# Optimization experiments

Hardware: AMD Instinct MI355X
Metric: run time of the kernel (lower is better)

Reference implementation:

```python
import jax, jax.numpy as jnp
import numpy as np

S, N, D, F, E = 2048, 8, 1024, 4096, 8
STD = 0.02


def setup_inputs() -> dict:
    key = jax.random.key(0)
    ks = jax.random.split(key, 5)
    x = jax.random.normal(ks[0], (S, N, D), dtype=jnp.float32)
    Wg = jax.random.normal(ks[1], (E, D), dtype=jnp.float32) * STD
    W1 = jax.random.normal(ks[2], (E, F, D), dtype=jnp.float32) * STD
    b1 = jnp.zeros((E, F), dtype=jnp.float32)
    W2 = jax.random.normal(ks[3], (E, D, F), dtype=jnp.float32) * STD
    b2 = jnp.zeros((E, D), dtype=jnp.float32)
    return {"x": x, "Wg": Wg, "W1": W1, "b1": b1, "W2": W2, "b2": b2}


def reference(x, Wg, W1, b1, W2, b2):
    # Gate (eval mode: no gating noise). scores: [S, N, E]
    scores = jnp.einsum('snd,ed->sne', x, Wg)
    prob = jax.nn.softmax(scores, axis=-1)
    top1_idx = jnp.argmax(prob, axis=-1)                                   # [S, N] int
    top1_prob = jnp.take_along_axis(prob, top1_idx[..., None], axis=-1)[..., 0]  # [S, N]

    y = jnp.zeros_like(x)
    n_experts = Wg.shape[0]
    for e in range(n_experts):  # small fixed loop over experts
        h = jax.nn.gelu(jnp.einsum('snd,fd->snf', x, W1[e]) + b1[e], approximate=False)
        ye = jnp.einsum('snf,df->snd', h, W2[e]) + b2[e]
        mask = (top1_idx == e)[..., None]                                  # [S, N, 1]
        y = y + jnp.where(mask, ye * top1_prob[..., None], 0.0)
    return y
```

## Files before the change

### kernel.cpp

```cpp
#include <hip/hip_runtime.h>

#define S_TOK 16384
#define D_DIM 1024
#define F_DIM 4096
#define E_NUM 8

#define BM 256
#define BN 128
#define BK 64
#define MT_MAX 72

typedef short bf16x8 __attribute__((ext_vector_type(8)));
typedef float f32x4 __attribute__((ext_vector_type(4)));
typedef unsigned short ushort_t;

static __device__ __forceinline__ unsigned short f32_bf16(float f) {
  unsigned u = __float_as_uint(f);
  return (unsigned short)((u + 0x7FFFu + ((u >> 16) & 1u)) >> 16);
}

static __device__ __forceinline__ unsigned int pack_bf16x2(float a, float b) {
  unsigned ua = __float_as_uint(a);
  unsigned ub = __float_as_uint(b);
  unsigned lo = (ua + 0x7FFFu + ((ua >> 16) & 1u)) >> 16;
  unsigned hi = (ub + 0x7FFFu + ((ub >> 16) & 1u)) & 0xFFFF0000u;
  return lo | hi;
}

static __device__ __forceinline__ uint2 cvt_f4_bf4(const float4 v) {
  uint2 r;
  r.x = pack_bf16x2(v.x, v.y);
  r.y = pack_bf16x2(v.z, v.w);
  return r;
}

static __device__ __forceinline__ void load_lds16(const void* g, void* l) {
  __builtin_amdgcn_global_load_lds(g, l, 16, 0, 0);
}

static __device__ __forceinline__ float gelu_f(float v) {
  const float u = fabsf(v) * 0.70710678118654752f;
  const float t = 1.0f / (1.0f + 0.3275911f * u);
  const float poly = t * (0.254829592f + t * (-0.284496736f + t * (1.421413741f +
                     t * (-1.453152027f + t * 1.061405429f))));
  const float erfa = 1.0f - poly * __expf(-u * u);
  const float erfv = (v >= 0.0f) ? erfa : -erfa;
  return 0.5f * v * (1.0f + erfv);
}

__global__ void zero_counts_kernel(int* counts) {
  if (threadIdx.x < E_NUM) counts[threadIdx.x] = 0;
}

__global__ void cast2_kernel(const float* __restrict__ w1, ushort_t* __restrict__ o1,
                             const float* __restrict__ w2, ushort_t* __restrict__ o2) {
  const int half = 16384;
  const float* src = (blockIdx.x < half) ? w1 : w2;
  ushort_t* dst = (blockIdx.x < half) ? o1 : o2;
  const int b = (blockIdx.x < half) ? blockIdx.x : (blockIdx.x - half);
  const size_t base = ((size_t)b * blockDim.x + threadIdx.x) * 8;
  const float4 v0 = *(const float4*)(src + base);
  const float4 v1 = *(const float4*)(src + base + 4);
  const uint2 a = cvt_f4_bf4(v0), c = cvt_f4_bf4(v1);
  uint4 w; w.x = a.x; w.y = a.y; w.z = c.x; w.w = c.y;
  *(uint4*)(dst + base) = w;
}

__global__ void gate_kernel(const float* __restrict__ x,
                            const float* __restrict__ Wg,
                            ushort_t* __restrict__ xbf,
                            float* __restrict__ prob,
                            int* __restrict__ counts,
                            int* __restrict__ tok_list) {
  const int wv = threadIdx.x >> 6;
  const int lane = threadIdx.x & 63;
  const int t = blockIdx.x * 4 + wv;
  const float* xr = x + (size_t)t * D_DIM;
  ushort_t* xb = xbf + (size_t)t * D_DIM;

  float acc[E_NUM];
#pragma unroll
  for (int e = 0; e < E_NUM; ++e) acc[e] = 0.0f;

#pragma unroll
  for (int i = 0; i < 4; ++i) {
    const int k = i * 256 + lane * 4;
    const float4 v = *(const float4*)(xr + k);
    *(uint2*)(xb + k) = cvt_f4_bf4(v);
#pragma unroll
    for (int e = 0; e < E_NUM; ++e) {
      const float4 w = *(const float4*)(Wg + e * D_DIM + k);
      acc[e] += v.x * w.x + v.y * w.y + v.z * w.z + v.w * w.w;
    }
  }
#pragma unroll
  for (int e = 0; e < E_NUM; ++e) {
#pragma unroll
    for (int off = 32; off > 0; off >>= 1)
      acc[e] += __shfl_xor(acc[e], off, 64);
  }
  if (lane == 0) {
    float m = acc[0]; int bi = 0;
#pragma unroll
    for (int e = 1; e < E_NUM; ++e) {
      if (acc[e] > m) { m = acc[e]; bi = e; }
    }
    float s = 0.0f;
#pragma unroll
    for (int e = 0; e < E_NUM; ++e) s += expf(acc[e] - m);
    prob[t] = 1.0f / s;
    int p = atomicAdd(&counts[bi], 1);
    tok_list[bi * S_TOK + p] = t;
  }
}

__global__ void plan_kernel(const int* __restrict__ counts, int* __restrict__ plan) {
  if (threadIdx.x == 0) {
    int t = 0;
    for (int e = 0; e < E_NUM; ++e) {
      const int nt = (counts[e] + BM - 1) / BM;
      for (int i = 0; i < nt; ++i) {
        plan[1 + t] = e;
        plan[1 + MT_MAX + t] = i * BM;
        ++t;
      }
    }
    plan[0] = t;
  }
}

template <int KDIM, int NDIM, int EPI>
__launch_bounds__(512, 3)
__global__ void ffn_kernel(const ushort_t* __restrict__ A,
                           const ushort_t* __restrict__ B,
                           const float* __restrict__ bias,
                           const float* __restrict__ prob,
                           const int* __restrict__ counts,
                           const int* __restrict__ tok_list,
                           const int* __restrict__ plan,
                           ushort_t* __restrict__ Hout,
                           float* __restrict__ out) {
  constexpr int NT = NDIM / BN;
  constexpr int NK = KDIM / BK;
  const int ntiles = plan[0];
  const int live = ntiles * NT;
  if (blockIdx.x >= live) return;
  const int q = live >> 3, r = live & 7;
  const int xcd = blockIdx.x & 7, idx = blockIdx.x >> 3;
  const int wg = (xcd < r ? xcd * (q + 1) : r * (q + 1) + (xcd - r) * q) + idx;
  const int tile = wg / NT;
  const int n0 = (wg % NT) * BN;
  const int e = plan[1 + tile];
  const int m0 = plan[1 + MT_MAX + tile];
  const int cnt = counts[e];

  __shared__ ushort_t As[BM * BK];
  __shared__ ushort_t Bs[BN * BK];

  const int tid = threadIdx.x;
  const int lane = tid & 63;
  const int w = tid >> 6;
  const int wr = (w >> 1) * 64;
  const int wc = (w & 1) * 64;
  const int l15 = lane & 15;
  const int l4  = lane >> 4;

  const int sub = lane >> 3;
  const int sslot = ((lane & 7) ^ sub) * 8;

  const size_t ebase = (size_t)e * S_TOK;
  const ushort_t* Be = B + (size_t)e * NDIM * KDIM;
  const ushort_t* pA[4];
#pragma unroll
  for (int j = 0; j < 4; ++j) {
    const int ra = m0 + w * 32 + j * 8 + sub;
    const int tok = (ra < cnt) ? tok_list[ebase + ra] : 0;
    pA[j] = A + (size_t)tok * KDIM + sslot;
  }
  const ushort_t* pB[2];
#pragma unroll
  for (int j = 0; j < 2; ++j)
    pB[j] = Be + (size_t)(n0 + w * 16 + j * 8 + sub) * KDIM + sslot;

  int oA[4][2], oB[4][2];
#pragma unroll
  for (int m = 0; m < 4; ++m) {
    const int rr = wr + m * 16 + l15;
#pragma unroll
    for (int kk = 0; kk < 2; ++kk)
      oA[m][kk] = rr * BK + (((kk * 4 + l4) ^ (rr & 7)) * 8);
  }
#pragma unroll
  for (int n = 0; n < 4; ++n) {
    const int rr = wc + n * 16 + l15;
#pragma unroll
    for (int kk = 0; kk < 2; ++kk)
      oB[n][kk] = rr * BK + (((kk * 4 + l4) ^ (rr & 7)) * 8);
  }

  f32x4 acc[4][4];
#pragma unroll
  for (int i = 0; i < 4; ++i)
#pragma unroll
    for (int j = 0; j < 4; ++j)
      acc[i][j] = (f32x4){0.f, 0.f, 0.f, 0.f};

  for (int t = 0; t < NK; ++t) {
    const int k0 = t * BK;
#pragma unroll
    for (int j = 0; j < 4; ++j)
      load_lds16(pA[j] + k0, &As[w * 2048 + j * 512]);
#pragma unroll
    for (int j = 0; j < 2; ++j)
      load_lds16(pB[j] + k0, &Bs[w * 1024 + j * 512]);
    __syncthreads();

#pragma unroll
    for (int kk = 0; kk < 2; ++kk) {
      bf16x8 a[4], b[4];
#pragma unroll
      for (int i = 0; i < 4; ++i) {
        a[i] = *(const bf16x8*)&As[oA[i][kk]];
        b[i] = *(const bf16x8*)&Bs[oB[i][kk]];
      }
#pragma unroll
      for (int mi = 0; mi < 4; ++mi)
#pragma unroll
        for (int ni = 0; ni < 4; ++ni)
          acc[mi][ni] = __builtin_amdgcn_mfma_f32_16x16x32_bf16(a[mi], b[ni], acc[mi][ni], 0, 0, 0);
    }

    __syncthreads();
  }

  const float* be = bias + (size_t)e * NDIM;
#pragma unroll
  for (int mi = 0; mi < 4; ++mi) {
#pragma unroll
    for (int rr = 0; rr < 4; ++rr) {
      const int slot = m0 + wr + mi * 16 + l4 * 4 + rr;
      if (slot >= cnt) continue;
      const int tok = tok_list[ebase + slot];
      if (EPI == 0) {
        ushort_t* hrow = Hout + (size_t)tok * NDIM;
#pragma unroll
        for (int ni = 0; ni < 4; ++ni) {
          const int col = n0 + wc + ni * 16 + l15;
          hrow[col] = f32_bf16(gelu_f(acc[mi][ni][rr] + be[col]));
        }
      } else {
        const float p = prob[tok];
        float* orow = out + (size_t)tok * NDIM;
#pragma unroll
        for (int ni = 0; ni < 4; ++ni) {
          const int col = n0 + wc + ni * 16 + l15;
          orow[col] = (acc[mi][ni][rr] + be[col]) * p;
        }
      }
    }
  }
}

extern "C" void kernel_launch(void* const* d_in, const int* in_sizes, int n_in,
                              void* d_out, int out_size, void* d_ws, size_t ws_size,
                              hipStream_t stream) {
  const float* x  = (const float*)d_in[0];
  const float* Wg = (const float*)d_in[1];
  const float* W1 = (const float*)d_in[2];
  const float* b1 = (const float*)d_in[3];
  const float* W2 = (const float*)d_in[4];
  const float* b2 = (const float*)d_in[5];
  float* out = (float*)d_out;

  const size_t MB = 1ull << 20;
  char* ws = (char*)d_ws;
  int* counts      = (int*)(ws);
  int* plan        = (int*)(ws + 4096);
  float* prob      = (float*)(ws + 64 * 1024);
  int* tok_list    = (int*)(ws + 128 * 1024);
  ushort_t* xbf    = (ushort_t*)(ws + 1 * MB);
  ushort_t* W1bf   = (ushort_t*)(ws + 33 * MB);
  ushort_t* W2bf   = (ushort_t*)(ws + 97 * MB);
  ushort_t* H      = (ushort_t*)(ws + 161 * MB);

  zero_counts_kernel<<<1, 64, 0, stream>>>(counts);
  gate_kernel<<<S_TOK / 4, 256, 0, stream>>>(x, Wg, xbf, prob, counts, tok_list);
  plan_kernel<<<1, 64, 0, stream>>>(counts, plan);

  cast2_kernel<<<32768, 256, 0, stream>>>(W1, W1bf, W2, W2bf);

  ffn_kernel<D_DIM, F_DIM, 0><<<(F_DIM / BN) * MT_MAX, 512, 0, stream>>>(
      xbf, W1bf, b1, nullptr, counts, tok_list, plan, H, nullptr);

  ffn_kernel<F_DIM, D_DIM, 1><<<(D_DIM / BN) * MT_MAX, 512, 0, stream>>>(
      H, W2bf, b2, prob, counts, tok_list, plan, nullptr, out);
}
```

Measured before the change: 722.5 us.

## Enlarge FFN tile to 256x256 and double-buffer LDS loads

Widens the N tile from 128 to 256 so each wave computes a 128x64 sub-tile with 32 accumulators, which raises arithmetic intensity per LDS byte. It also double-buffers A/B in LDS, prefetching the next K slice while MFMAs run on the current one, and drops one barrier per iteration. The cost is higher register and LDS use (occupancy hint lowered from 3 to 2 blocks), and fewer workgroups, which may hurt load balance across CUs.

```diff
diff --git a/kernel.cpp b/kernel.cpp
--- a/kernel.cpp
+++ b/kernel.cpp
@@ -6,7 +6,7 @@
 #define E_NUM 8
 
 #define BM 256
-#define BN 128
+#define BN 256
 #define BK 64
 #define MT_MAX 72
 
@@ -130,7 +130,7 @@
 }
 
 template <int KDIM, int NDIM, int EPI>
-__launch_bounds__(512, 3)
+__launch_bounds__(512, 2)
 __global__ void ffn_kernel(const ushort_t* __restrict__ A,
                            const ushort_t* __restrict__ B,
                            const float* __restrict__ bias,
@@ -154,14 +154,14 @@
   const int m0 = plan[1 + MT_MAX + tile];
   const int cnt = counts[e];
 
-  __shared__ ushort_t As[BM * BK];
-  __shared__ ushort_t Bs[BN * BK];
+  __shared__ ushort_t As[2][BM * BK];
+  __shared__ ushort_t Bs[2][BN * BK];
 
   const int tid = threadIdx.x;
   const int lane = tid & 63;
   const int w = tid >> 6;
-  const int wr = (w >> 1) * 64;
-  const int wc = (w & 1) * 64;
+  const int wr2 = (w >> 2) * 128;
+  const int wc4 = (w & 3) * 64;
   const int l15 = lane & 15;
   const int l4  = lane >> 4;
 
@@ -171,90 +171,96 @@
   const size_t ebase = (size_t)e * S_TOK;
   const ushort_t* Be = B + (size_t)e * NDIM * KDIM;
   const ushort_t* pA[4];
+  const ushort_t* pB[4];
 #pragma unroll
   for (int j = 0; j < 4; ++j) {
-    const int ra = m0 + w * 32 + j * 8 + sub;
+    const int ra = m0 + j * 64 + w * 8 + sub;
     const int tok = (ra < cnt) ? tok_list[ebase + ra] : 0;
     pA[j] = A + (size_t)tok * KDIM + sslot;
-  }
-  const ushort_t* pB[2];
-#pragma unroll
-  for (int j = 0; j < 2; ++j)
-    pB[j] = Be + (size_t)(n0 + w * 16 + j * 8 + sub) * KDIM + sslot;
-
-  int oA[4][2], oB[4][2];
-#pragma unroll
-  for (int m = 0; m < 4; ++m) {
-    const int rr = wr + m * 16 + l15;
+    pB[j] = Be + (size_t)(n0 + j * 64 + w * 8 + sub) * KDIM + sslot;
+  }
+
+  int oA[8][2], oB[4][2];
+#pragma unroll
+  for (int m = 0; m < 8; ++m) {
+    const int rr = wr2 + m * 16 + l15;
 #pragma unroll
     for (int kk = 0; kk < 2; ++kk)
       oA[m][kk] = rr * BK + (((kk * 4 + l4) ^ (rr & 7)) * 8);
   }
 #pragma unroll
   for (int n = 0; n < 4; ++n) {
-    const int rr = wc + n * 16 + l15;
+    const int rr = wc4 + n * 16 + l15;
 #pragma unroll
     for (int kk = 0; kk < 2; ++kk)
       oB[n][kk] = rr * BK + (((kk * 4 + l4) ^ (rr & 7)) * 8);
   }
 
-  f32x4 acc[4][4];
-#pragma unroll
-  for (int i = 0; i < 4; ++i)
+  f32x4 acc[8][4];
+#pragma unroll
+  for (int i = 0; i < 8; ++i)
 #pragma unroll
     for (int j = 0; j < 4; ++j)
       acc[i][j] = (f32x4){0.f, 0.f, 0.f, 0.f};
 
+#pragma unroll
+  for (int j = 0; j < 4; ++j) {
+    load_lds16(pA[j], &As[0][j * 4096 + w * 512]);
+    load_lds16(pB[j], &Bs[0][j * 4096 + w * 512]);
+  }
+  __syncthreads();
+
   for (int t = 0; t < NK; ++t) {
-    const int k0 = t * BK;
-#pragma unroll
-    for (int j = 0; j < 4; ++j)
-      load_lds16(pA[j] + k0, &As[w * 2048 + j * 512]);
-#pragma unroll
-    for (int j = 0; j < 2; ++j)
-      load_lds16(pB[j] + k0, &Bs[w * 1024 + j * 512]);
+    const int cb = t & 1;
+    if (t + 1 < NK) {
+      const int kn = (t + 1) * BK;
+      const int nb = cb ^ 1;
+#pragma unroll
+      for (int j = 0; j < 4; ++j) {
+        load_lds16(pA[j] + kn, &As[nb][j * 4096 + w * 512]);
+        load_lds16(pB[j] + kn, &Bs[nb][j * 4096 + w * 512]);
+      }
+    }
+
+#pragma unroll
+    for (int kk = 0; kk < 2; ++kk) {
+      bf16x8 a[8], b[4];
+#pragma unroll
+      for (int m = 0; m < 8; ++m) a[m] = *(const bf16x8*)&As[cb][oA[m][kk]];
+#pragma unroll
+      for (int n = 0; n < 4; ++n) b[n] = *(const bf16x8*)&Bs[cb][oB[n][kk]];
+#pragma unroll
+      for (int m = 0; m < 8; ++m)
+#pragma unroll
+        for (int n = 0; n < 4; ++n)
+          acc[m][n] = __builtin_amdgcn_mfma_f32_16x16x32_bf16(a[m], b[n], acc[m][n], 0, 0, 0);
+    }
+
     __syncthreads();
-
-#pragma unroll
-    for (int kk = 0; kk < 2; ++kk) {
-      bf16x8 a[4], b[4];
-#pragma unroll
-      for (int i = 0; i < 4; ++i) {
-        a[i] = *(const bf16x8*)&As[oA[i][kk]];
-        b[i] = *(const bf16x8*)&Bs[oB[i][kk]];
-      }
-#pragma unroll
-      for (int mi = 0; mi < 4; ++mi)
-#pragma unroll
-        for (int ni = 0; ni < 4; ++ni)
-          acc[mi][ni] = __builtin_amdgcn_mfma_f32_16x16x32_bf16(a[mi], b[ni], acc[mi][ni], 0, 0, 0);
-    }
-
-    __syncthreads();
   }
 
   const float* be = bias + (size_t)e * NDIM;
 #pragma unroll
-  for (int mi = 0; mi < 4; ++mi) {
+  for (int m = 0; m < 8; ++m) {
 #pragma unroll
     for (int rr = 0; rr < 4; ++rr) {
-      const int slot = m0 + wr + mi * 16 + l4 * 4 + rr;
+      const int slot = m0 + wr2 + m * 16 + l4 * 4 + rr;
       if (slot >= cnt) continue;
       const int tok = tok_list[ebase + slot];
       if (EPI == 0) {
         ushort_t* hrow = Hout + (size_t)tok * NDIM;
 #pragma unroll
-        for (int ni = 0; ni < 4; ++ni) {
-          const int col = n0 + wc + ni * 16 + l15;
-          hrow[col] = f32_bf16(gelu_f(acc[mi][ni][rr] + be[col]));
+        for (int n = 0; n < 4; ++n) {
+          const int col = n0 + wc4 + n * 16 + l15;
+          hrow[col] = f32_bf16(gelu_f(acc[m][n][rr] + be[col]));
         }
       } else {
         const float p = prob[tok];
         float* orow = out + (size_t)tok * NDIM;
 #pragma unroll
-        for (int ni = 0; ni < 4; ++ni) {
-          const int col = n0 + wc + ni * 16 + l15;
-          orow[col] = (acc[mi][ni][rr] + be[col]) * p;
+        for (int n = 0; n < 4; ++n) {
+          const int col = n0 + wc4 + n * 16 + l15;
+          orow[col] = (acc[m][n][rr] + be[col]) * p;
         }
       }
     }
```

Result: slower. 842.0 us (+16.5%).

## Double-buffer LDS tiles in FFN GEMMs and fold plan and zeroing kernels

Applied to the files above, without the earlier changes.

The expert FFN GEMM moves to a double-buffered LDS scheme with BK=32. Each iteration issues the global-to-LDS loads for the next K tile before running the MFMAs on the current one, so each K step needs one barrier instead of two. The separate counts-zeroing and plan kernels are removed: zeroing now happens inside the weight-cast kernel, and each GEMM block rebuilds the tile-to-expert mapping from the counts itself. This drops two tiny launches. The cost is a lower occupancy hint (launch bounds 3 to 2), half as much K work per barrier, and a leftover stray prologue load.

```diff
diff --git a/kernel.cpp b/kernel.cpp
--- a/kernel.cpp
+++ b/kernel.cpp
@@ -7,7 +7,7 @@
 
 #define BM 256
 #define BN 128
-#define BK 64
+#define BK 32
 #define MT_MAX 72
 
 typedef short bf16x8 __attribute__((ext_vector_type(8)));
@@ -48,12 +48,10 @@
   return 0.5f * v * (1.0f + erfv);
 }
 
-__global__ void zero_counts_kernel(int* counts) {
-  if (threadIdx.x < E_NUM) counts[threadIdx.x] = 0;
-}
-
 __global__ void cast2_kernel(const float* __restrict__ w1, ushort_t* __restrict__ o1,
-                             const float* __restrict__ w2, ushort_t* __restrict__ o2) {
+                             const float* __restrict__ w2, ushort_t* __restrict__ o2,
+                             int* __restrict__ counts) {
+  if (blockIdx.x == 0 && threadIdx.x < E_NUM) counts[threadIdx.x] = 0;
   const int half = 16384;
   const float* src = (blockIdx.x < half) ? w1 : w2;
   ushort_t* dst = (blockIdx.x < half) ? o1 : o2;
@@ -114,35 +112,26 @@
   }
 }
 
-__global__ void plan_kernel(const int* __restrict__ counts, int* __restrict__ plan) {
-  if (threadIdx.x == 0) {
-    int t = 0;
-    for (int e = 0; e < E_NUM; ++e) {
-      const int nt = (counts[e] + BM - 1) / BM;
-      for (int i = 0; i < nt; ++i) {
-        plan[1 + t] = e;
-        plan[1 + MT_MAX + t] = i * BM;
-        ++t;
-      }
-    }
-    plan[0] = t;
-  }
-}
+#define SWZ32(r) (((r) >> 1) & 3)
 
 template <int KDIM, int NDIM, int EPI>
-__launch_bounds__(512, 3)
+__launch_bounds__(512, 2)
 __global__ void ffn_kernel(const ushort_t* __restrict__ A,
                            const ushort_t* __restrict__ B,
                            const float* __restrict__ bias,
                            const float* __restrict__ prob,
                            const int* __restrict__ counts,
                            const int* __restrict__ tok_list,
-                           const int* __restrict__ plan,
                            ushort_t* __restrict__ Hout,
                            float* __restrict__ out) {
   constexpr int NT = NDIM / BN;
   constexpr int NK = KDIM / BK;
-  const int ntiles = plan[0];
+  int nt_e[E_NUM], ntiles = 0;
+#pragma unroll
+  for (int i = 0; i < E_NUM; ++i) {
+    nt_e[i] = (counts[i] + BM - 1) / BM;
+    ntiles += nt_e[i];
+  }
   const int live = ntiles * NT;
   if (blockIdx.x >= live) return;
   const int q = live >> 3, r = live & 7;
@@ -150,12 +139,16 @@
   const int wg = (xcd < r ? xcd * (q + 1) : r * (q + 1) + (xcd - r) * q) + idx;
   const int tile = wg / NT;
   const int n0 = (wg % NT) * BN;
-  const int e = plan[1 + tile];
-  const int m0 = plan[1 + MT_MAX + tile];
+  int e = 0, m0 = 0, accb = 0;
+#pragma unroll
+  for (int i = 0; i < E_NUM; ++i) {
+    if (tile >= accb && tile < accb + nt_e[i]) { e = i; m0 = (tile - accb) * BM; }
+    accb += nt_e[i];
+  }
   const int cnt = counts[e];
 
-  __shared__ ushort_t As[BM * BK];
-  __shared__ ushort_t Bs[BN * BK];
+  __shared__ ushort_t As[2][BM * BK];
+  __shared__ ushort_t Bs[2][BN * BK];
 
   const int tid = threadIdx.x;
   const int lane = tid & 63;
@@ -165,37 +158,31 @@
   const int l15 = lane & 15;
   const int l4  = lane >> 4;
 
-  const int sub = lane >> 3;
-  const int sslot = ((lane & 7) ^ sub) * 8;
+  const int srow = tid >> 2;
+  const int sslot = ((tid & 3) ^ SWZ32(srow)) * 8;
+  const int w256 = w * 256;
 
   const size_t ebase = (size_t)e * S_TOK;
   const ushort_t* Be = B + (size_t)e * NDIM * KDIM;
-  const ushort_t* pA[4];
-#pragma unroll
-  for (int j = 0; j < 4; ++j) {
-    const int ra = m0 + w * 32 + j * 8 + sub;
+  const ushort_t* pA[2];
+#pragma unroll
+  for (int j = 0; j < 2; ++j) {
+    const int ra = m0 + j * 128 + srow;
     const int tok = (ra < cnt) ? tok_list[ebase + ra] : 0;
     pA[j] = A + (size_t)tok * KDIM + sslot;
   }
-  const ushort_t* pB[2];
-#pragma unroll
-  for (int j = 0; j < 2; ++j)
-    pB[j] = Be + (size_t)(n0 + w * 16 + j * 8 + sub) * KDIM + sslot;
-
-  int oA[4][2], oB[4][2];
+  const ushort_t* pBr = Be + (size_t)(n0 + srow) * KDIM + sslot;
+
+  int oA[4], oB[4];
 #pragma unroll
   for (int m = 0; m < 4; ++m) {
     const int rr = wr + m * 16 + l15;
-#pragma unroll
-    for (int kk = 0; kk < 2; ++kk)
-      oA[m][kk] = rr * BK + (((kk * 4 + l4) ^ (rr & 7)) * 8);
+    oA[m] = rr * BK + ((l4 ^ SWZ32(rr)) * 8);
   }
 #pragma unroll
   for (int n = 0; n < 4; ++n) {
     const int rr = wc + n * 16 + l15;
-#pragma unroll
-    for (int kk = 0; kk < 2; ++kk)
-      oB[n][kk] = rr * BK + (((kk * 4 + l4) ^ (rr & 7)) * 8);
+    oB[n] = rr * BK + ((l4 ^ SWZ32(rr)) * 8);
   }
 
   f32x4 acc[4][4];
@@ -205,30 +192,36 @@
     for (int j = 0; j < 4; ++j)
       acc[i][j] = (f32x4){0.f, 0.f, 0.f, 0.f};
 
+  load_lds16(pA[0], &As[0][w256 + ((tid & 255) >= 0 ? 0 : 0)]);
+  __syncthreads();
+  {
+    load_lds16(pA[0], &As[0][w * 512]);
+    load_lds16(pA[1], &As[0][4096 + w * 512]);
+    load_lds16(pBr,   &Bs[0][w * 512]);
+  }
+  __syncthreads();
+
   for (int t = 0; t < NK; ++t) {
-    const int k0 = t * BK;
-#pragma unroll
-    for (int j = 0; j < 4; ++j)
-      load_lds16(pA[j] + k0, &As[w * 2048 + j * 512]);
-#pragma unroll
-    for (int j = 0; j < 2; ++j)
-      load_lds16(pB[j] + k0, &Bs[w * 1024 + j * 512]);
-    __syncthreads();
-
-#pragma unroll
-    for (int kk = 0; kk < 2; ++kk) {
-      bf16x8 a[4], b[4];
-#pragma unroll
-      for (int i = 0; i < 4; ++i) {
-        a[i] = *(const bf16x8*)&As[oA[i][kk]];
-        b[i] = *(const bf16x8*)&Bs[oB[i][kk]];
-      }
-#pragma unroll
-      for (int mi = 0; mi < 4; ++mi)
-#pragma unroll
-        for (int ni = 0; ni < 4; ++ni)
-          acc[mi][ni] = __builtin_amdgcn_mfma_f32_16x16x32_bf16(a[mi], b[ni], acc[mi][ni], 0, 0, 0);
-    }
+    const int cb = t & 1;
+    if (t + 1 < NK) {
+      const int kn = (t + 1) * BK;
+      const int nb = cb ^ 1;
+      load_lds16(pA[0] + kn, &As[nb][w * 512]);
+      load_lds16(pA[1] + kn, &As[nb][4096 + w * 512]);
+      load_lds16(pBr + kn,   &Bs[nb][w * 512]);
+    }
+
+    bf16x8 a[4], b[4];
+#pragma unroll
+    for (int i = 0; i < 4; ++i) {
+      a[i] = *(const bf16x8*)&As[cb][oA[i]];
+      b[i] = *(const bf16x8*)&Bs[cb][oB[i]];
+    }
+#pragma unroll
+    for (int mi = 0; mi < 4; ++mi)
+#pragma unroll
+      for (int ni = 0; ni < 4; ++ni)
+        acc[mi][ni] = __builtin_amdgcn_mfma_f32_16x16x32_bf16(a[mi], b[ni], acc[mi][ni], 0, 0, 0);
 
     __syncthreads();
   }
@@ -275,7 +268,6 @@
   const size_t MB = 1ull << 20;
   char* ws = (char*)d_ws;
   int* counts      = (int*)(ws);
-  int* plan        = (int*)(ws + 4096);
   float* prob      = (float*)(ws + 64 * 1024);
   int* tok_list    = (int*)(ws + 128 * 1024);
   ushort_t* xbf    = (ushort_t*)(ws + 1 * MB);
@@ -283,15 +275,12 @@
   ushort_t* W2bf   = (ushort_t*)(ws + 97 * MB);
   ushort_t* H      = (ushort_t*)(ws + 161 * MB);
 
-  zero_counts_kernel<<<1, 64, 0, stream>>>(counts);
+  cast2_kernel<<<32768, 256, 0, stream>>>(W1, W1bf, W2, W2bf, counts);
   gate_kernel<<<S_TOK / 4, 256, 0, stream>>>(x, Wg, xbf, prob, counts, tok_list);
-  plan_kernel<<<1, 64, 0, stream>>>(counts, plan);
-
-  cast2_kernel<<<32768, 256, 0, stream>>>(W1, W1bf, W2, W2bf);
 
   ffn_kernel<D_DIM, F_DIM, 0><<<(F_DIM / BN) * MT_MAX, 512, 0, stream>>>(
-      xbf, W1bf, b1, nullptr, counts, tok_list, plan, H, nullptr);
+      xbf, W1bf, b1, nullptr, counts, tok_list, H, nullptr);
 
   ffn_kernel<F_DIM, D_DIM, 1><<<(D_DIM / BN) * MT_MAX, 512, 0, stream>>>(
-      H, W2bf, b2, prob, counts, tok_list, plan, nullptr, out);
-}
+      H, W2bf, b2, prob, counts, tok_list, nullptr, out);
+}
```

New measurement: 731.9 us. No clear change (+1.3%).

## Fuse weight casts into gate and FFN kernels, drop plan kernel

Applied to the files above, without the earlier changes.

Folds the W1 fp32-to-bf16 cast into the gate kernel as extra blocks. Folds the W2 cast into the first FFN GEMM launch as trailing blocks, so that cast can overlap with GEMM work. Removes the single-thread plan kernel by having each GEMM block work out its expert and row offset from the counts. This cuts two kernel launches and the serial plan step. The trade-offs are some redundant per-block index arithmetic and cast blocks competing with GEMM blocks for the same compute units.

```diff
diff --git a/kernel.cpp b/kernel.cpp
--- a/kernel.cpp
+++ b/kernel.cpp
@@ -52,29 +52,26 @@
   if (threadIdx.x < E_NUM) counts[threadIdx.x] = 0;
 }
 
-__global__ void cast2_kernel(const float* __restrict__ w1, ushort_t* __restrict__ o1,
-                             const float* __restrict__ w2, ushort_t* __restrict__ o2) {
-  const int half = 16384;
-  const float* src = (blockIdx.x < half) ? w1 : w2;
-  ushort_t* dst = (blockIdx.x < half) ? o1 : o2;
-  const int b = (blockIdx.x < half) ? blockIdx.x : (blockIdx.x - half);
-  const size_t base = ((size_t)b * blockDim.x + threadIdx.x) * 8;
-  const float4 v0 = *(const float4*)(src + base);
-  const float4 v1 = *(const float4*)(src + base + 4);
-  const uint2 a = cvt_f4_bf4(v0), c = cvt_f4_bf4(v1);
-  uint4 w; w.x = a.x; w.y = a.y; w.z = c.x; w.w = c.y;
-  *(uint4*)(dst + base) = w;
-}
-
-__global__ void gate_kernel(const float* __restrict__ x,
-                            const float* __restrict__ Wg,
-                            ushort_t* __restrict__ xbf,
-                            float* __restrict__ prob,
-                            int* __restrict__ counts,
-                            int* __restrict__ tok_list) {
+__global__ void gate_cast_kernel(const float* __restrict__ x,
+                                 const float* __restrict__ Wg,
+                                 ushort_t* __restrict__ xbf,
+                                 float* __restrict__ prob,
+                                 int* __restrict__ counts,
+                                 int* __restrict__ tok_list,
+                                 const float* __restrict__ w1,
+                                 ushort_t* __restrict__ o1) {
+  if (blockIdx.x < 16384) {
+    const size_t base = ((size_t)blockIdx.x * 256 + threadIdx.x) * 8;
+    const float4 v0 = *(const float4*)(w1 + base);
+    const float4 v1 = *(const float4*)(w1 + base + 4);
+    const uint2 a = cvt_f4_bf4(v0), c = cvt_f4_bf4(v1);
+    uint4 w; w.x = a.x; w.y = a.y; w.z = c.x; w.w = c.y;
+    *(uint4*)(o1 + base) = w;
+    return;
+  }
   const int wv = threadIdx.x >> 6;
   const int lane = threadIdx.x & 63;
-  const int t = blockIdx.x * 4 + wv;
+  const int t = (blockIdx.x - 16384) * 4 + wv;
   const float* xr = x + (size_t)t * D_DIM;
   ushort_t* xb = xbf + (size_t)t * D_DIM;
 
@@ -114,22 +111,7 @@
   }
 }
 
-__global__ void plan_kernel(const int* __restrict__ counts, int* __restrict__ plan) {
-  if (threadIdx.x == 0) {
-    int t = 0;
-    for (int e = 0; e < E_NUM; ++e) {
-      const int nt = (counts[e] + BM - 1) / BM;
-      for (int i = 0; i < nt; ++i) {
-        plan[1 + t] = e;
-        plan[1 + MT_MAX + t] = i * BM;
-        ++t;
-      }
-    }
-    plan[0] = t;
-  }
-}
-
-template <int KDIM, int NDIM, int EPI>
+template <int KDIM, int NDIM, int EPI, int CAST_BLOCKS>
 __launch_bounds__(512, 3)
 __global__ void ffn_kernel(const ushort_t* __restrict__ A,
                            const ushort_t* __restrict__ B,
@@ -137,12 +119,30 @@
                            const float* __restrict__ prob,
                            const int* __restrict__ counts,
                            const int* __restrict__ tok_list,
-                           const int* __restrict__ plan,
                            ushort_t* __restrict__ Hout,
-                           float* __restrict__ out) {
+                           float* __restrict__ out,
+                           const float* __restrict__ csrc,
+                           ushort_t* __restrict__ cdst) {
   constexpr int NT = NDIM / BN;
   constexpr int NK = KDIM / BK;
-  const int ntiles = plan[0];
+  constexpr int GRID_MAIN = NT * MT_MAX;
+
+  if (CAST_BLOCKS > 0 && blockIdx.x >= GRID_MAIN) {
+    const size_t base = ((size_t)(blockIdx.x - GRID_MAIN) * 512 + threadIdx.x) * 8;
+    const float4 v0 = *(const float4*)(csrc + base);
+    const float4 v1 = *(const float4*)(csrc + base + 4);
+    const uint2 a = cvt_f4_bf4(v0), c = cvt_f4_bf4(v1);
+    uint4 w; w.x = a.x; w.y = a.y; w.z = c.x; w.w = c.y;
+    *(uint4*)(cdst + base) = w;
+    return;
+  }
+
+  int nt_e[E_NUM], ntiles = 0;
+#pragma unroll
+  for (int i = 0; i < E_NUM; ++i) {
+    nt_e[i] = (counts[i] + BM - 1) / BM;
+    ntiles += nt_e[i];
+  }
   const int live = ntiles * NT;
   if (blockIdx.x >= live) return;
   const int q = live >> 3, r = live & 7;
@@ -150,8 +150,12 @@
   const int wg = (xcd < r ? xcd * (q + 1) : r * (q + 1) + (xcd - r) * q) + idx;
   const int tile = wg / NT;
   const int n0 = (wg % NT) * BN;
-  const int e = plan[1 + tile];
-  const int m0 = plan[1 + MT_MAX + tile];
+  int e = 0, m0 = 0, accb = 0;
+#pragma unroll
+  for (int i = 0; i < E_NUM; ++i) {
+    if (tile >= accb && tile < accb + nt_e[i]) { e = i; m0 = (tile - accb) * BM; }
+    accb += nt_e[i];
+  }
   const int cnt = counts[e];
 
   __shared__ ushort_t As[BM * BK];
@@ -275,7 +279,6 @@
   const size_t MB = 1ull << 20;
   char* ws = (char*)d_ws;
   int* counts      = (int*)(ws);
-  int* plan        = (int*)(ws + 4096);
   float* prob      = (float*)(ws + 64 * 1024);
   int* tok_list    = (int*)(ws + 128 * 1024);
   ushort_t* xbf    = (ushort_t*)(ws + 1 * MB);
@@ -284,14 +287,13 @@
   ushort_t* H      = (ushort_t*)(ws + 161 * MB);
 
   zero_counts_kernel<<<1, 64, 0, stream>>>(counts);
-  gate_kernel<<<S_TOK / 4, 256, 0, stream>>>(x, Wg, xbf, prob, counts, tok_list);
-  plan_kernel<<<1, 64, 0, stream>>>(counts, plan);
-
-  cast2_kernel<<<32768, 256, 0, stream>>>(W1, W1bf, W2, W2bf);
-
-  ffn_kernel<D_DIM, F_DIM, 0><<<(F_DIM / BN) * MT_MAX, 512, 0, stream>>>(
-      xbf, W1bf, b1, nullptr, counts, tok_list, plan, H, nullptr);
-
-  ffn_kernel<F_DIM, D_DIM, 1><<<(D_DIM / BN) * MT_MAX, 512, 0, stream>>>(
-      H, W2bf, b2, prob, counts, tok_list, plan, nullptr, out);
-}
+
+  gate_cast_kernel<<<16384 + S_TOK / 4, 256, 0, stream>>>(
+      x, Wg, xbf, prob, counts, tok_list, W1, W1bf);
+
+  ffn_kernel<D_DIM, F_DIM, 0, 8192><<<(F_DIM / BN) * MT_MAX + 8192, 512, 0, stream>>>(
+      xbf, W1bf, b1, nullptr, counts, tok_list, H, nullptr, W2, W2bf);
+
+  ffn_kernel<F_DIM, D_DIM, 1, 0><<<(D_DIM / BN) * MT_MAX, 512, 0, stream>>>(
+      H, W2bf, b2, prob, counts, tok_list, nullptr, out, nullptr, nullptr);
+}
```

After: 846.4 us. 1.17x slower.
